# Kernel tuning notes

Measured on AMD Instinct MI355X. Metric: run time of the kernel, lower is better.

Reference implementation:

```python
import jax, jax.numpy as jnp
import numpy as np

E = 200      # embsize
R = 480      # num relations
T = 8        # cur_ts (history length)
N = 40000    # num entities
B = 1024     # batch of triples
NEG_INF = -1.0e9


def _lin(x, W, b):
    # torch nn.Linear convention: y = x @ W.T + b
    return x @ W.T + b


def _gru_cell(x, h, wih, whh, bih, bhh):
    # torch GRUCell: gates packed as [r, z, n]
    gi = x @ wih.T + bih
    gh = h @ whh.T + bhh
    i_r, i_z, i_n = jnp.split(gi, 3, axis=1)
    h_r, h_z, h_n = jnp.split(gh, 3, axis=1)
    r = jax.nn.sigmoid(i_r + h_r)
    z = jax.nn.sigmoid(i_z + h_z)
    n = jnp.tanh(i_n + r * h_n)
    return (1.0 - z) * n + z * h


def setup_inputs() -> dict:
    key = jax.random.key(0)
    ks = jax.random.split(key, 24)
    s = 0.05
    pre_emb = jax.random.normal(ks[0], (N, E), dtype=jnp.float32)
    r_emb = jax.random.normal(ks[1], (R, E), dtype=jnp.float32)
    partial_embeding = jax.random.randint(ks[2], (B, T * R), 0, 2).astype(jnp.float32)
    sub = jax.random.randint(ks[3], (B,), 0, N)
    rel = jax.random.randint(ks[4], (B,), 0, R)
    obj = jax.random.randint(ks[5], (B,), 0, N)
    all_triples = jnp.stack([sub, rel, obj], axis=1).astype(jnp.int64)
    params = {
        'W1': jax.random.normal(ks[6], (2 * E, E)) * s, 'b1': jnp.zeros((2 * E,)),
        'W2': jax.random.normal(ks[7], (E, 2 * E)) * s, 'b2': jnp.zeros((E,)),
        'Wa': jax.random.normal(ks[8], (E, E)) * s, 'ba': jnp.zeros((E,)),
        'Wh1': jax.random.normal(ks[9], (E, E)) * s, 'bh1': jnp.zeros((E,)),
        'Wh2': jax.random.normal(ks[10], (E, E)) * s, 'bh2': jnp.zeros((E,)),
        'Wal': jax.random.normal(ks[11], (E, E)) * s, 'bal': jnp.zeros((E,)),
        'gru_wih': jax.random.normal(ks[12], (3 * E, E)) * s,
        'gru_whh': jax.random.normal(ks[13], (3 * E, E)) * s,
        'gru_bih': jnp.zeros((3 * E,)),
        'gru_bhh': jnp.zeros((3 * E,)),
    }
    params = {k: v.astype(jnp.float32) for k, v in params.items()}
    out = {'pre_emb': pre_emb, 'r_emb': r_emb, 'partial_embeding': partial_embeding,
           'all_triples': all_triples, 'cur_ts': T, 'num_rel': R}
    out.update(params)
    return out


def reference(pre_emb, r_emb, partial_embeding, all_triples, cur_ts, num_rel,
              W1, b1, W2, b2, Wa, ba, Wh1, bh1, Wh2, bh2, Wal, bal,
              gru_wih, gru_whh, gru_bih, gru_bhh):
    mapped_rel = _lin(_lin(r_emb, W1, b1), W2, b2)          # [R, E]
    q_rel = mapped_rel[all_triples[:, 1]]                    # [B, E]
    b = partial_embeding.shape[0]

    # loop-invariant attention base: linear_attn(q_rel) @ mapped_rel^T -> [B, R]
    base = _lin(q_rel, Wa, ba) @ mapped_rel.T

    # [B, cur_ts*R] -> [cur_ts, B, R] for scan over timesteps
    pe = partial_embeding.reshape(b, cur_ts, num_rel).transpose(1, 0, 2)

    def step(h, cur):
        attn = cur * base
        attn = jnp.where(attn == 0, jnp.float32(NEG_INF), attn)
        a = jax.nn.softmax(attn, axis=1)
        x = a @ mapped_rel                                   # [B, E]
        h = _gru_cell(x, h, gru_wih, gru_whh, gru_bih, gru_bhh)
        return h, None

    h0 = jnp.zeros((b, mapped_rel.shape[1]), dtype=pre_emb.dtype)
    gru_hidden, _ = jax.lax.scan(step, h0, pe)

    predicted_hist = 0.1 * _lin(_lin(q_rel, Wh1, bh1), Wh2, bh2) + q_rel
    match_loss = jnp.mean((predicted_hist - gru_hidden) ** 2)

    # forward_forth (distmult scoring)
    gru_hidden2 = _gru_cell(q_rel, predicted_hist, gru_wih, gru_whh, gru_bih, gru_bhh)
    sub_emb = pre_emb[all_triples[:, 0]]
    score_logits = (_lin(sub_emb, Wal, bal) * gru_hidden2) @ _lin(pre_emb, Wal, bal).T  # [B, N]
    score = jax.nn.sigmoid(score_logits)

    labels = jnp.zeros_like(score_logits).at[jnp.arange(b), all_triples[:, 2]].set(1.0)
    # stable BCE(sigmoid(s), y)
    path_loss = -jnp.mean(labels * jax.nn.log_sigmoid(score_logits)
                          + (1.0 - labels) * jax.nn.log_sigmoid(-score_logits))
    return (match_loss, path_loss, score)
```

## Files before the change

kernel.cpp:

```cpp
#include <hip/hip_runtime.h>
#include <hip/hip_bf16.h>
#include <math.h>

#define EE 200
#define RR 480
#define TT 8
#define NN 40000
#define BB 1024
#define KP 224
#define GP 672
#define GPR 704
#define LDS_STRIDE 232
#define SPAN 800

typedef __attribute__((ext_vector_type(8))) short short8v;
typedef __attribute__((ext_vector_type(4))) float f32x4;

__device__ inline unsigned short f2bf(float x) {
    unsigned int u = __float_as_uint(x);
    unsigned int r = ((u >> 16) & 1u) + 0x7fffu;
    return (unsigned short)((u + r) >> 16);
}
__device__ inline float bf2f(unsigned short h) {
    return __uint_as_float(((unsigned int)h) << 16);
}
__device__ inline float sigm(float x) { return 1.0f / (1.0f + __expf(-x)); }
__device__ inline void split_store(unsigned short* hi, unsigned short* lo, size_t i, float v) {
    unsigned short h = f2bf(v);
    hi[i] = h;
    lo[i] = f2bf(v - bf2f(h));
}

struct PrepPtrs {
    unsigned short *W1h, *W1l, *W2h, *W2l, *Wabh, *Wabl, *Wh2h, *Wh2l;
    unsigned short *Walh, *Wall, *WTh, *WTl, *wgh, *wgl, *whg, *whl;
    float *bab, *bihp, *bhhp;
    unsigned short *mapSh, *mapSl, *wgiSh, *wgiSl, *hbufs;
    double* acc;
};

__global__ __launch_bounds__(256) void prep_kernel(
    const float* __restrict__ W1, const float* __restrict__ W2,
    const float* __restrict__ Wa, const float* __restrict__ Wh1,
    const float* __restrict__ Wh2, const float* __restrict__ Wal,
    const float* __restrict__ bal, const float* __restrict__ wih,
    const float* __restrict__ whh, const float* __restrict__ ba,
    const float* __restrict__ bh1, const float* __restrict__ bih,
    const float* __restrict__ bhh, PrepPtrs p)
{
    const int gt = blockIdx.x * 256 + threadIdx.x;
    const int gs = gridDim.x * 256;

    for (int i = gt; i < 448 * 224; i += gs) {
        int r = i / 224, c = i - r * 224;
        split_store(p.W1h, p.W1l, i, (r < 400 && c < 200) ? W1[r * 200 + c] : 0.f);
        float vab = 0.f;
        if (c < 200) {
            if (r < 200) vab = Wa[r * 200 + c];
            else if (r >= 224 && r < 424) vab = Wh1[(r - 224) * 200 + c];
        }
        split_store(p.Wabh, p.Wabl, i, vab);
    }
    for (int i = gt; i < 256 * 416; i += gs) {
        int r = i / 416, c = i - r * 416;
        split_store(p.W2h, p.W2l, i, (r < 200 && c < 400) ? W2[r * 400 + c] : 0.f);
    }
    for (int i = gt; i < 256 * 224; i += gs) {
        int r = i / 224, c = i - r * 224;
        bool in = (r < 200 && c < 200);
        split_store(p.Wh2h, p.Wh2l, i, in ? Wh2[r * 200 + c] : 0.f);
        split_store(p.Walh, p.Wall, i, in ? Wal[r * 200 + c] : 0.f);
        float vt = in ? Wal[c * 200 + r] : ((r == 200 && c < 200) ? bal[c] : 0.f);
        split_store(p.WTh, p.WTl, i, vt);
    }
    for (int i = gt; i < 672 * 224; i += gs) {
        int rr = i / 224, c = i - rr * 224;
        int g = rr / 224, j = rr - g * 224;
        bool in = (j < 200 && c < 200);
        split_store(p.wgh, p.wgl, i, in ? wih[(size_t)(g * 200 + j) * 200 + c] : 0.f);
        split_store(p.whg, p.whl, i, in ? whh[(size_t)(g * 200 + j) * 200 + c] : 0.f);
    }
    for (int i = gt; i < 448; i += gs) {
        float v = 0.f;
        if (i < 200) v = ba[i];
        else if (i >= 224 && i < 424) v = bh1[i - 224];
        p.bab[i] = v;
    }
    for (int i = gt; i < GPR; i += gs) {
        int g = i / 224, j = i - g * 224;
        p.bihp[i] = (g < 3 && j < 200) ? bih[g * 200 + j] : 0.f;
    }
    for (int i = gt; i < GP; i += gs) {
        int g = i / 224, j = i - g * 224;
        p.bhhp[i] = (j < 200) ? bhh[g * 200 + j] : 0.f;
    }
    for (int i = gt; i < 512 * 224; i += gs) { p.mapSh[i] = 0; p.mapSl[i] = 0; }
    for (int i = gt; i < 704 * 480; i += gs) { p.wgiSh[i] = 0; p.wgiSl[i] = 0; }
    for (int i = gt; i < 4 * BB * KP; i += gs) p.hbufs[i] = 0;
    if (gt == 0) { p.acc[0] = 0.0; p.acc[1] = 0.0; }
}

template <int MODE, int OUT, int GATHER, int GATEPAD, int EGATHER>
__global__ __launch_bounds__(256) void mfma_flyA(
    const float* __restrict__ A, int lda, const int* __restrict__ gidx, int gsel,
    const unsigned short* __restrict__ Bhi, const unsigned short* __restrict__ Blo,
    const float* __restrict__ bias,
    float* __restrict__ Cf, unsigned short* __restrict__ Chi, unsigned short* __restrict__ Clo,
    int M, int N, int Ka, int Ks,
    const float* __restrict__ extra, int eld, float alpha, int obf)
{
    const int tid = threadIdx.x;
    const int wave = tid >> 6, lane = tid & 63;
    const int r16 = lane & 15, kq = lane >> 4;
    const int kbase = kq * 8;
    const int bm = blockIdx.y * 64 + wave * 16;
    const int bn = blockIdx.x * 64;

    int arow = bm + r16;
    const bool avalid = arow < M;
    if (GATHER) { if (avalid) arow = gidx[arow * 3 + gsel]; }
    const float* Ap = A + (size_t)arow * lda;

    f32x4 acc[4] = {{0,0,0,0},{0,0,0,0},{0,0,0,0},{0,0,0,0}};
    const int nk = Ks >> 5;

    for (int kk = 0; kk < nk; kk++) {
        const int k0 = kk * 32 + kbase;
        short8v a0, a1;
        #pragma unroll
        for (int e = 0; e < 8; e++) {
            float v = (avalid && (k0 + e) < Ka) ? Ap[k0 + e] : 0.f;
            unsigned short h = f2bf(v);
            a0[e] = (short)h;
            a1[e] = (short)f2bf(v - bf2f(h));
        }
        #pragma unroll
        for (int nf = 0; nf < 4; nf++) {
            const size_t boff = (size_t)(bn + nf * 16 + r16) * Ks + k0;
            short8v b0 = *(const short8v*)(Bhi + boff);
            short8v b1 = *(const short8v*)(Blo + boff);
            acc[nf] = __builtin_amdgcn_mfma_f32_16x16x32_bf16(a0, b1, acc[nf], 0, 0, 0);
            acc[nf] = __builtin_amdgcn_mfma_f32_16x16x32_bf16(a1, b0, acc[nf], 0, 0, 0);
            acc[nf] = __builtin_amdgcn_mfma_f32_16x16x32_bf16(a0, b0, acc[nf], 0, 0, 0);
        }
    }

    #pragma unroll
    for (int r = 0; r < 4; r++) {
        const int orow = bm + kq * 4 + r;
        if (orow >= M) continue;
        #pragma unroll
        for (int nf = 0; nf < 4; nf++) {
            const int col = bn + nf * 16 + r16;
            float v = acc[nf][r];
            if (OUT == 0) {
                if (col < N) {
                    if (bias) v += bias[col];
                    if (MODE == 1) {
                        float ex = EGATHER ? extra[(size_t)gidx[orow * 3 + gsel] * eld + col]
                                           : extra[(size_t)orow * eld + col];
                        v = alpha * v + ex;
                    } else if (MODE == 2) {
                        v = v * extra[(size_t)orow * eld + col];
                    }
                    Cf[(size_t)orow * N + col] = v;
                }
            } else if (OUT == 1) {
                if (col < obf) {
                    float w = 0.f;
                    if (col < N) { w = v; if (bias) w += bias[col]; }
                    Chi[(size_t)orow * obf + col] = f2bf(w);
                }
            } else if (OUT == 2) {
                if (col < N) {
                    int wr = GATEPAD ? (orow / 200) * 224 + orow % 200 : orow;
                    if (bias) v += bias[col];
                    split_store(Chi, Clo, (size_t)wr * obf + col, v);
                }
            } else if (OUT == 3) {
                if (col < N) {
                    if (bias) v += bias[col];
                    Cf[(size_t)orow * N + col] = v;
                    split_store(Chi, Clo, (size_t)orow * obf + col, v);
                }
            }
        }
    }
}

__global__ __launch_bounds__(256) void mfma_linear1_kernel(
    const unsigned short* __restrict__ Ahi,
    const unsigned short* __restrict__ Bhi,
    const float* __restrict__ bias, float* __restrict__ C,
    int M, int N, int Ks)
{
    const int tid  = threadIdx.x;
    const int wave = tid >> 6;
    const int lane = tid & 63;
    const int r16   = lane & 15;
    const int khalf = lane >> 4;
    const int kbase = khalf * 8;
    const int bm = blockIdx.y * 64 + wave * 16;
    const int bn = blockIdx.x * 64;

    const unsigned short* ah = Ahi + (size_t)(bm + r16) * Ks + kbase;
    const unsigned short* bh = Bhi + (size_t)(bn + r16) * Ks + kbase;

    f32x4 acc[4] = {{0,0,0,0},{0,0,0,0},{0,0,0,0},{0,0,0,0}};

    for (int k0 = 0; k0 < Ks; k0 += 32) {
        short8v a0 = *(const short8v*)(ah + k0);
        #pragma unroll
        for (int nf = 0; nf < 4; nf++) {
            short8v b0 = *(const short8v*)(bh + (size_t)nf * 16 * Ks + k0);
            acc[nf] = __builtin_amdgcn_mfma_f32_16x16x32_bf16(a0, b0, acc[nf], 0, 0, 0);
        }
    }
    #pragma unroll
    for (int r = 0; r < 4; r++) {
        const int row = bm + khalf * 4 + r;
        #pragma unroll
        for (int nf = 0; nf < 4; nf++) {
            const int col = bn + nf * 16 + r16;
            if (col < N)
                C[(size_t)row * N + col] = acc[nf][r] + (bias ? bias[col] : 0.0f);
        }
    }
}

template <int FIRST, int LAST>
__global__ __launch_bounds__(256) void gru_step_kernel(
    const unsigned short* __restrict__ Whi, const unsigned short* __restrict__ Wlo,
    const float* __restrict__ bhh_pad,
    const float* __restrict__ gi_t,
    const unsigned short* __restrict__ hin_hi, const unsigned short* __restrict__ hin_lo,
    unsigned short* __restrict__ hout_hi, unsigned short* __restrict__ hout_lo,
    float* __restrict__ h_fin)
{
    const int tid = threadIdx.x;
    const int wave = tid >> 6, lane = tid & 63;
    const int r16 = lane & 15, kq = lane >> 4;
    const int jf = blockIdx.x;
    const int brow = (blockIdx.y * 4 + wave) * 16;
    const int j = jf * 16 + r16;

    f32x4 ar = {0,0,0,0}, az = {0,0,0,0}, an = {0,0,0,0};
    if (!FIRST) {
        short8v ahi[7], alo[7];
        const unsigned short* hh = hin_hi + (size_t)(brow + r16) * KP + kq * 8;
        const unsigned short* hl = hin_lo + (size_t)(brow + r16) * KP + kq * 8;
        #pragma unroll
        for (int kk = 0; kk < 7; kk++) {
            ahi[kk] = *(const short8v*)(hh + kk * 32);
            alo[kk] = *(const short8v*)(hl + kk * 32);
        }
        #pragma unroll
        for (int kk = 0; kk < 7; kk++) {
            const size_t rowr = (size_t)(jf * 16 + r16) * KP + kk * 32 + kq * 8;
            const size_t rowz = rowr + (size_t)224 * KP;
            const size_t rown = rowr + (size_t)448 * KP;
            short8v brh = *(const short8v*)(Whi + rowr);
            short8v brl = *(const short8v*)(Wlo + rowr);
            short8v bzh = *(const short8v*)(Whi + rowz);
            short8v bzl = *(const short8v*)(Wlo + rowz);
            short8v bnh = *(const short8v*)(Whi + rown);
            short8v bnl = *(const short8v*)(Wlo + rown);
            ar = __builtin_amdgcn_mfma_f32_16x16x32_bf16(ahi[kk], brl, ar, 0, 0, 0);
            az = __builtin_amdgcn_mfma_f32_16x16x32_bf16(ahi[kk], bzl, az, 0, 0, 0);
            an = __builtin_amdgcn_mfma_f32_16x16x32_bf16(ahi[kk], bnl, an, 0, 0, 0);
            ar = __builtin_amdgcn_mfma_f32_16x16x32_bf16(alo[kk], brh, ar, 0, 0, 0);
            az = __builtin_amdgcn_mfma_f32_16x16x32_bf16(alo[kk], bzh, az, 0, 0, 0);
            an = __builtin_amdgcn_mfma_f32_16x16x32_bf16(alo[kk], bnh, an, 0, 0, 0);
            ar = __builtin_amdgcn_mfma_f32_16x16x32_bf16(ahi[kk], brh, ar, 0, 0, 0);
            az = __builtin_amdgcn_mfma_f32_16x16x32_bf16(ahi[kk], bzh, az, 0, 0, 0);
            an = __builtin_amdgcn_mfma_f32_16x16x32_bf16(ahi[kk], bnh, an, 0, 0, 0);
        }
    }

    const float br = bhh_pad[j], bz = bhh_pad[224 + j], bn_ = bhh_pad[448 + j];
    #pragma unroll
    for (int q = 0; q < 4; q++) {
        const int row = brow + kq * 4 + q;
        float gir = gi_t[(size_t)row * GP + j];
        float giz = gi_t[(size_t)row * GP + 224 + j];
        float gin = gi_t[(size_t)row * GP + 448 + j];
        float r_ = sigm(gir + ar[q] + br);
        float z_ = sigm(giz + az[q] + bz);
        float n_ = tanhf(gin + r_ * (an[q] + bn_));
        float hold = 0.0f;
        if (!FIRST)
            hold = bf2f(hin_hi[(size_t)row * KP + j]) + bf2f(hin_lo[(size_t)row * KP + j]);
        float hnew = (1.0f - z_) * n_ + z_ * hold;
        if (j < EE) {
            unsigned short nh = f2bf(hnew);
            hout_hi[(size_t)row * KP + j] = nh;
            hout_lo[(size_t)row * KP + j] = f2bf(hnew - bf2f(nh));
            if (LAST) h_fin[(size_t)row * EE + j] = hnew;
        }
    }
}

__global__ __launch_bounds__(256) void gru2_fused_kernel(
    const unsigned short* __restrict__ Wihi, const unsigned short* __restrict__ Wilo,
    const unsigned short* __restrict__ Whhi, const unsigned short* __restrict__ Whlo,
    const float* __restrict__ bih_pad, const float* __restrict__ bhh_pad,
    const int* __restrict__ triples, const float* __restrict__ map,
    const float* __restrict__ hp, const float* __restrict__ hfin,
    float* __restrict__ ghid2, double* __restrict__ accMatch)
{
    __shared__ float red[256];
    const int tid = threadIdx.x;
    const int wave = tid >> 6, lane = tid & 63;
    const int r16 = lane & 15, kq = lane >> 4;
    const int jf = blockIdx.x;
    const int brow = (blockIdx.y * 4 + wave) * 16;
    const int j = jf * 16 + r16;

    f32x4 ir = {0,0,0,0}, iz = {0,0,0,0}, in_ = {0,0,0,0};
    f32x4 hr = {0,0,0,0}, hz = {0,0,0,0}, hn = {0,0,0,0};

    {
        const int xrow = triples[(brow + r16) * 3 + 1];
        const float* xp = map + (size_t)xrow * EE;
        #pragma unroll
        for (int kk = 0; kk < 7; kk++) {
            short8v a0, a1;
            #pragma unroll
            for (int e = 0; e < 8; e++) {
                int k = kk * 32 + kq * 8 + e;
                float v = (k < EE) ? xp[k] : 0.0f;
                unsigned short hhh = f2bf(v);
                a0[e] = (short)hhh;
                a1[e] = (short)f2bf(v - bf2f(hhh));
            }
            const size_t rowr = (size_t)(jf * 16 + r16) * KP + kk * 32 + kq * 8;
            const size_t rowz = rowr + (size_t)224 * KP;
            const size_t rown = rowr + (size_t)448 * KP;
            short8v brh = *(const short8v*)(Wihi + rowr);
            short8v brl = *(const short8v*)(Wilo + rowr);
            short8v bzh = *(const short8v*)(Wihi + rowz);
            short8v bzl = *(const short8v*)(Wilo + rowz);
            short8v bnh = *(const short8v*)(Wihi + rown);
            short8v bnl = *(const short8v*)(Wilo + rown);
            ir = __builtin_amdgcn_mfma_f32_16x16x32_bf16(a0, brl, ir, 0, 0, 0);
            iz = __builtin_amdgcn_mfma_f32_16x16x32_bf16(a0, bzl, iz, 0, 0, 0);
            in_ = __builtin_amdgcn_mfma_f32_16x16x32_bf16(a0, bnl, in_, 0, 0, 0);
            ir = __builtin_amdgcn_mfma_f32_16x16x32_bf16(a1, brh, ir, 0, 0, 0);
            iz = __builtin_amdgcn_mfma_f32_16x16x32_bf16(a1, bzh, iz, 0, 0, 0);
            in_ = __builtin_amdgcn_mfma_f32_16x16x32_bf16(a1, bnh, in_, 0, 0, 0);
            ir = __builtin_amdgcn_mfma_f32_16x16x32_bf16(a0, brh, ir, 0, 0, 0);
            iz = __builtin_amdgcn_mfma_f32_16x16x32_bf16(a0, bzh, iz, 0, 0, 0);
            in_ = __builtin_amdgcn_mfma_f32_16x16x32_bf16(a0, bnh, in_, 0, 0, 0);
        }
    }
    {
        const float* hpp = hp + (size_t)(brow + r16) * EE;
        #pragma unroll
        for (int kk = 0; kk < 7; kk++) {
            short8v a0, a1;
            #pragma unroll
            for (int e = 0; e < 8; e++) {
                int k = kk * 32 + kq * 8 + e;
                float v = (k < EE) ? hpp[k] : 0.0f;
                unsigned short hhh = f2bf(v);
                a0[e] = (short)hhh;
                a1[e] = (short)f2bf(v - bf2f(hhh));
            }
            const size_t rowr = (size_t)(jf * 16 + r16) * KP + kk * 32 + kq * 8;
            const size_t rowz = rowr + (size_t)224 * KP;
            const size_t rown = rowr + (size_t)448 * KP;
            short8v brh = *(const short8v*)(Whhi + rowr);
            short8v brl = *(const short8v*)(Whlo + rowr);
            short8v bzh = *(const short8v*)(Whhi + rowz);
            short8v bzl = *(const short8v*)(Whlo + rowz);
            short8v bnh = *(const short8v*)(Whhi + rown);
            short8v bnl = *(const short8v*)(Whlo + rown);
            hr = __builtin_amdgcn_mfma_f32_16x16x32_bf16(a0, brl, hr, 0, 0, 0);
            hz = __builtin_amdgcn_mfma_f32_16x16x32_bf16(a0, bzl, hz, 0, 0, 0);
            hn = __builtin_amdgcn_mfma_f32_16x16x32_bf16(a0, bnl, hn, 0, 0, 0);
            hr = __builtin_amdgcn_mfma_f32_16x16x32_bf16(a1, brh, hr, 0, 0, 0);
            hz = __builtin_amdgcn_mfma_f32_16x16x32_bf16(a1, bzh, hz, 0, 0, 0);
            hn = __builtin_amdgcn_mfma_f32_16x16x32_bf16(a1, bnh, hn, 0, 0, 0);
            hr = __builtin_amdgcn_mfma_f32_16x16x32_bf16(a0, brh, hr, 0, 0, 0);
            hz = __builtin_amdgcn_mfma_f32_16x16x32_bf16(a0, bzh, hz, 0, 0, 0);
            hn = __builtin_amdgcn_mfma_f32_16x16x32_bf16(a0, bnh, hn, 0, 0, 0);
        }
    }

    float psum = 0.0f;
    if (j < EE) {
        const float bir = bih_pad[j], biz = bih_pad[224 + j], bin = bih_pad[448 + j];
        const float bhr = bhh_pad[j], bhz = bhh_pad[224 + j], bhn = bhh_pad[448 + j];
        #pragma unroll
        for (int q = 0; q < 4; q++) {
            const int row = brow + kq * 4 + q;
            float r_ = sigm(ir[q] + bir + hr[q] + bhr);
            float z_ = sigm(iz[q] + biz + hz[q] + bhz);
            float n_ = tanhf(in_[q] + bin + r_ * (hn[q] + bhn));
            float hold = hp[(size_t)row * EE + j];
            ghid2[(size_t)row * EE + j] = (1.0f - z_) * n_ + z_ * hold;
            float d = hold - hfin[(size_t)row * EE + j];
            psum += d * d;
        }
    }
    red[tid] = psum;
    __syncthreads();
    for (int s = 128; s > 0; s >>= 1) {
        if (tid < s) red[tid] += red[tid + s];
        __syncthreads();
    }
    if (tid == 0) atomicAdd(accMatch, (double)red[0]);
}

__global__ __launch_bounds__(256) void score_mfma3_kernel(
    const unsigned short* __restrict__ Ubf,
    const float* __restrict__ pre_emb,
    const int* __restrict__ triples,
    float* __restrict__ outScore,
    double* __restrict__ accPath)
{
    __shared__ unsigned short Bs[32 * LDS_STRIDE];
    __shared__ int objs[64];
    __shared__ float red[256];

    const int tid = threadIdx.x;
    const int wave = tid >> 6, lane = tid & 63;
    const int r16 = lane & 15, khalf = lane >> 4;
    const int kbase = khalf * 8;
    const int colbase = blockIdx.x * SPAN;
    const int mbase = blockIdx.y * 64;
    const int m0 = mbase + wave * 16;

    if (tid < 64) objs[tid] = triples[(mbase + tid) * 3 + 2];
    for (int idx = tid; idx < 32 * 24; idx += 256) {
        int row = idx / 24;
        int cc = idx - row * 24;
        Bs[row * LDS_STRIDE + 200 + cc] = (cc == 0) ? (unsigned short)0x3F80 : (unsigned short)0;
    }

    short8v a[7];
    {
        const unsigned short* Ap = Ubf + (size_t)(m0 + r16) * KP + kbase;
        #pragma unroll
        for (int kk = 0; kk < 7; kk++) a[kk] = *(const short8v*)(Ap + kk * 32);
    }

    float psum = 0.0f;

    for (int cj = 0; cj < SPAN / 32; cj++) {
        const int bn = colbase + cj * 32;
        __syncthreads();
        for (int idx = tid; idx < 32 * 50; idx += 256) {
            int row = idx / 50;
            int c4 = (idx - row * 50) * 4;
            float4 v = *(const float4*)(pre_emb + (size_t)(bn + row) * EE + c4);
            unsigned short* d = &Bs[row * LDS_STRIDE + c4];
            d[0] = f2bf(v.x); d[1] = f2bf(v.y); d[2] = f2bf(v.z); d[3] = f2bf(v.w);
        }
        __syncthreads();

        f32x4 acc0 = {0,0,0,0}, acc1 = {0,0,0,0};
        #pragma unroll
        for (int kk = 0; kk < 7; kk++) {
            short8v b0 = *(const short8v*)&Bs[( 0 + r16) * LDS_STRIDE + kk * 32 + kbase];
            short8v b1 = *(const short8v*)&Bs[(16 + r16) * LDS_STRIDE + kk * 32 + kbase];
            acc0 = __builtin_amdgcn_mfma_f32_16x16x32_bf16(a[kk], b0, acc0, 0, 0, 0);
            acc1 = __builtin_amdgcn_mfma_f32_16x16x32_bf16(a[kk], b1, acc1, 0, 0, 0);
        }
        #pragma unroll
        for (int r = 0; r < 4; r++) {
            const int grow = m0 + khalf * 4 + r;
            const int objc = objs[grow - mbase];
            float xv[2] = { acc0[r], acc1[r] };
            #pragma unroll
            for (int nf = 0; nf < 2; nf++) {
                const int col = bn + nf * 16 + r16;
                float x  = xv[nf];
                float e  = __expf(-fabsf(x));
                float t1 = 1.0f + e;
                float rc = __builtin_amdgcn_rcpf(t1);
                float sig = (x >= 0.0f) ? rc : e * rc;
                float sp = __logf(t1);
                float s  = (col == objc) ? x : -x;
                psum += fminf(s, 0.0f) - sp;
                outScore[(size_t)grow * NN + col] = sig;
            }
        }
    }
    red[tid] = psum;
    __syncthreads();
    for (int s = 128; s > 0; s >>= 1) {
        if (tid < s) red[tid] += red[tid + s];
        __syncthreads();
    }
    if (tid == 0) atomicAdd(accPath, (double)red[0]);
}

__global__ __launch_bounds__(256) void masked_softmax_all_kernel(
    const float* __restrict__ base, const float* __restrict__ part,
    unsigned short* __restrict__ aout_hi)
{
    __shared__ float sv[RR];
    __shared__ float red[256];
    const int blk = blockIdx.x;
    const int b = blk & (BB - 1);
    const int t = blk >> 10;
    const int tid = threadIdx.x;
    const float* brow = base + (size_t)b * RR;
    const float* prow = part + (size_t)b * (TT * RR) + t * RR;

    float lmax = -3.0e38f;
    for (int r = tid; r < RR; r += 256) {
        float v = prow[r] * brow[r];
        if (v == 0.0f) v = -1000000000.0f;
        sv[r] = v;
        lmax = fmaxf(lmax, v);
    }
    red[tid] = lmax;
    __syncthreads();
    for (int s = 128; s > 0; s >>= 1) {
        if (tid < s) red[tid] = fmaxf(red[tid], red[tid + s]);
        __syncthreads();
    }
    float gmax = red[0];
    __syncthreads();

    float lsum = 0.0f;
    for (int r = tid; r < RR; r += 256) {
        float e = __expf(sv[r] - gmax);
        sv[r] = e;
        lsum += e;
    }
    red[tid] = lsum;
    __syncthreads();
    for (int s = 128; s > 0; s >>= 1) {
        if (tid < s) red[tid] += red[tid + s];
        __syncthreads();
    }
    float inv = 1.0f / red[0];
    for (int r = tid; r < RR; r += 256)
        aout_hi[(size_t)blk * RR + r] = f2bf(sv[r] * inv);
}

__global__ void final_kernel(const double* __restrict__ acc, float* __restrict__ out)
{
    if (threadIdx.x == 0) {
        out[0] = (float)(acc[0] / ((double)BB * EE));
        out[1] = (float)(-acc[1] / ((double)BB * NN));
    }
}

extern "C" void kernel_launch(void* const* d_in, const int* in_sizes, int n_in,
                              void* d_out, int out_size, void* d_ws, size_t ws_size,
                              hipStream_t stream) {
    const float* pre_emb = (const float*)d_in[0];
    const float* r_emb   = (const float*)d_in[1];
    const float* part    = (const float*)d_in[2];
    const int*   triples = (const int*)d_in[3];
    const float* W1  = (const float*)d_in[6];
    const float* b1  = (const float*)d_in[7];
    const float* W2  = (const float*)d_in[8];
    const float* b2  = (const float*)d_in[9];
    const float* Wa  = (const float*)d_in[10];
    const float* ba  = (const float*)d_in[11];
    const float* Wh1 = (const float*)d_in[12];
    const float* bh1 = (const float*)d_in[13];
    const float* Wh2 = (const float*)d_in[14];
    const float* bh2 = (const float*)d_in[15];
    const float* Wal = (const float*)d_in[16];
    const float* bal = (const float*)d_in[17];
    const float* wih = (const float*)d_in[18];
    const float* whh = (const float*)d_in[19];
    const float* bih = (const float*)d_in[20];
    const float* bhh = (const float*)d_in[21];

    float* out = (float*)d_out;
    double* acc = (double*)d_ws;
    float* wsf = (float*)d_ws;
    size_t off = 4;
    auto alloc = [&](size_t n) { float* p = wsf + off; off += (n + 3) & ~(size_t)3; return p; };
    auto allocS = [&](size_t n) { return (unsigned short*)alloc((n + 1) / 2); };

    PrepPtrs p;
    p.W1h  = allocS((size_t)448 * 224);
    p.W1l  = allocS((size_t)448 * 224);
    p.W2h  = allocS((size_t)256 * 416);
    p.W2l  = allocS((size_t)256 * 416);
    p.Wabh = allocS((size_t)448 * 224);
    p.Wabl = allocS((size_t)448 * 224);
    p.Wh2h = allocS((size_t)256 * 224);
    p.Wh2l = allocS((size_t)256 * 224);
    p.Walh = allocS((size_t)256 * 224);
    p.Wall = allocS((size_t)256 * 224);
    p.WTh  = allocS((size_t)256 * 224);
    p.WTl  = allocS((size_t)256 * 224);
    p.wgh  = allocS((size_t)GP * KP);
    p.wgl  = allocS((size_t)GP * KP);
    p.whg  = allocS((size_t)GP * KP);
    p.whl  = allocS((size_t)GP * KP);
    p.bab  = alloc(448);
    p.bihp = alloc(GPR);
    p.bhhp = alloc(GP);
    p.mapSh = allocS((size_t)512 * 224);
    p.mapSl = allocS((size_t)512 * 224);
    p.wgiSh = allocS((size_t)GPR * RR);
    p.wgiSl = allocS((size_t)GPR * RR);
    p.hbufs = allocS((size_t)4 * BB * KP);
    p.acc = acc;

    unsigned short* ha_hi = p.hbufs;
    unsigned short* ha_lo = p.hbufs + (size_t)BB * KP;
    unsigned short* hb_hi = p.hbufs + (size_t)2 * BB * KP;
    unsigned short* hb_lo = p.hbufs + (size_t)3 * BB * KP;

    float* h1     = alloc((size_t)RR * 400);
    float* map    = alloc((size_t)RR * EE);
    float* qa_ph1 = alloc((size_t)BB * 448);
    float* basep  = alloc((size_t)BB * RR);
    unsigned short* aw_hi = allocS((size_t)TT * BB * RR);
    float* gi_all = alloc((size_t)TT * BB * GP);
    float* hfin   = alloc((size_t)BB * EE);
    float* pred   = alloc((size_t)BB * EE);
    float* ghid2  = alloc((size_t)BB * EE);
    float* s1h    = alloc((size_t)BB * EE);
    unsigned short* u_bf = allocS((size_t)BB * KP);

    dim3 blk(256);

    prep_kernel<<<1024, blk, 0, stream>>>(
        W1, W2, Wa, Wh1, Wh2, Wal, bal, wih, whh, ba, bh1, bih, bhh, p);

    mfma_flyA<0,0,0,0,0><<<dim3(7, 8), blk, 0, stream>>>(
        r_emb, 200, nullptr, 0, p.W1h, p.W1l, b1, h1, nullptr, nullptr,
        RR, 400, 200, 224, nullptr, 0, 0.f, 0);
    mfma_flyA<0,3,0,0,0><<<dim3(4, 8), blk, 0, stream>>>(
        h1, 400, nullptr, 0, p.W2h, p.W2l, b2, map, p.mapSh, p.mapSl,
        RR, EE, 400, 416, nullptr, 0, 0.f, 224);
    mfma_flyA<0,0,1,0,0><<<dim3(7, 16), blk, 0, stream>>>(
        map, 200, triples, 1, p.Wabh, p.Wabl, p.bab, qa_ph1, nullptr, nullptr,
        BB, 448, 200, 224, nullptr, 0, 0.f, 0);
    mfma_flyA<0,0,0,0,0><<<dim3(8, 16), blk, 0, stream>>>(
        qa_ph1, 448, nullptr, 0, p.mapSh, p.mapSl, nullptr, basep, nullptr, nullptr,
        BB, RR, 200, 224, nullptr, 0, 0.f, 0);
    masked_softmax_all_kernel<<<TT * BB, blk, 0, stream>>>(basep, part, aw_hi);
    mfma_flyA<0,2,0,1,0><<<dim3(8, 10), blk, 0, stream>>>(
        wih, 200, nullptr, 0, p.mapSh, p.mapSl, nullptr, nullptr, p.wgiSh, p.wgiSl,
        600, RR, 200, 224, nullptr, 0, 0.f, RR);
    mfma_linear1_kernel<<<dim3(11, TT * BB / 64), blk, 0, stream>>>(
        aw_hi, p.wgiSh, p.bihp, gi_all, TT * BB, GP, RR);

    for (int t = 0; t < TT; t++) {
        const float* gi_t = gi_all + (size_t)t * BB * GP;
        const unsigned short* ih = (t & 1) ? hb_hi : ha_hi;
        const unsigned short* il = (t & 1) ? hb_lo : ha_lo;
        unsigned short* oh = (t & 1) ? ha_hi : hb_hi;
        unsigned short* ol = (t & 1) ? ha_lo : hb_lo;
        if (t == 0)
            gru_step_kernel<1,0><<<dim3(13, BB / 64), blk, 0, stream>>>(
                p.whg, p.whl, p.bhhp, gi_t, ih, il, oh, ol, nullptr);
        else if (t == TT - 1)
            gru_step_kernel<0,1><<<dim3(13, BB / 64), blk, 0, stream>>>(
                p.whg, p.whl, p.bhhp, gi_t, ih, il, oh, ol, hfin);
        else
            gru_step_kernel<0,0><<<dim3(13, BB / 64), blk, 0, stream>>>(
                p.whg, p.whl, p.bhhp, gi_t, ih, il, oh, ol, nullptr);
    }

    mfma_flyA<1,0,0,0,1><<<dim3(4, 16), blk, 0, stream>>>(
        qa_ph1 + 224, 448, triples, 1, p.Wh2h, p.Wh2l, bh2, pred, nullptr, nullptr,
        BB, EE, 200, 224, map, 200, 0.1f, 0);
    gru2_fused_kernel<<<dim3(13, BB / 64), blk, 0, stream>>>(
        p.wgh, p.wgl, p.whg, p.whl, p.bihp, p.bhhp,
        triples, map, pred, hfin, ghid2, acc + 0);
    mfma_flyA<2,0,1,0,0><<<dim3(4, 16), blk, 0, stream>>>(
        pre_emb, 200, triples, 0, p.Walh, p.Wall, bal, s1h, nullptr, nullptr,
        BB, EE, 200, 224, ghid2, 200, 0.f, 0);
    mfma_flyA<0,1,0,0,0><<<dim3(4, 16), blk, 0, stream>>>(
        s1h, 200, nullptr, 0, p.WTh, p.WTl, nullptr, nullptr, u_bf, nullptr,
        BB, KP, 200, 224, nullptr, 0, 0.f, KP);
    score_mfma3_kernel<<<dim3(50, 16), blk, 0, stream>>>(u_bf, pre_emb, triples, out + 2, acc + 1);
    final_kernel<<<1, 64, 0, stream>>>(acc, out);
}
```

Baseline: 457.2 us.

## Swap MFMA operand roles in score kernel to write rows with float4 stores

The score GEMM kernel is restructured so pre_emb rows become the A operand, loaded straight from global memory and converted to bf16 in registers instead of being staged through LDS. U becomes the B operand, held in registers. The transposed output layout lets each lane store four consecutive columns of its own row as one float4, which is meant to improve write coalescing on the large 1024x40000 score output. LDS staging and the per-tile barriers are removed and the grid doubles. The trade-off is that pre_emb is now read redundantly by every wave with no LDS sharing, and each block covers a shorter column span.

After: 581.4 us. 1.27x slower.

```diff
diff --git a/kernel.cpp b/kernel.cpp
--- a/kernel.cpp
+++ b/kernel.cpp
@@ -10,8 +10,6 @@
 #define KP 224
 #define GP 672
 #define GPR 704
-#define LDS_STRIDE 232
-#define SPAN 800
 
 typedef __attribute__((ext_vector_type(8))) short short8v;
 typedef __attribute__((ext_vector_type(4))) float f32x4;
@@ -412,81 +410,77 @@
     if (tid == 0) atomicAdd(accMatch, (double)red[0]);
 }
 
-__global__ __launch_bounds__(256) void score_mfma3_kernel(
+__global__ __launch_bounds__(256) void score_mfma4_kernel(
     const unsigned short* __restrict__ Ubf,
     const float* __restrict__ pre_emb,
     const int* __restrict__ triples,
     float* __restrict__ outScore,
     double* __restrict__ accPath)
 {
-    __shared__ unsigned short Bs[32 * LDS_STRIDE];
-    __shared__ int objs[64];
     __shared__ float red[256];
-
     const int tid = threadIdx.x;
     const int wave = tid >> 6, lane = tid & 63;
-    const int r16 = lane & 15, khalf = lane >> 4;
-    const int kbase = khalf * 8;
-    const int colbase = blockIdx.x * SPAN;
-    const int mbase = blockIdx.y * 64;
-    const int m0 = mbase + wave * 16;
-
-    if (tid < 64) objs[tid] = triples[(mbase + tid) * 3 + 2];
-    for (int idx = tid; idx < 32 * 24; idx += 256) {
-        int row = idx / 24;
-        int cc = idx - row * 24;
-        Bs[row * LDS_STRIDE + 200 + cc] = (cc == 0) ? (unsigned short)0x3F80 : (unsigned short)0;
-    }
-
-    short8v a[7];
+    const int r16 = lane & 15, kq = lane >> 4;
+    const int kbase = kq * 8;
+    const int pc = blockIdx.x * 400;
+    const int u0 = blockIdx.y * 64 + wave * 16;
+
+    short8v bU[7];
     {
-        const unsigned short* Ap = Ubf + (size_t)(m0 + r16) * KP + kbase;
-        #pragma unroll
-        for (int kk = 0; kk < 7; kk++) a[kk] = *(const short8v*)(Ap + kk * 32);
-    }
+        const unsigned short* Up = Ubf + (size_t)(u0 + r16) * KP + kbase;
+        #pragma unroll
+        for (int kk = 0; kk < 7; kk++) bU[kk] = *(const short8v*)(Up + kk * 32);
+    }
+    const int myUrow = u0 + r16;
+    const int objc = triples[myUrow * 3 + 2];
 
     float psum = 0.0f;
 
-    for (int cj = 0; cj < SPAN / 32; cj++) {
-        const int bn = colbase + cj * 32;
-        __syncthreads();
-        for (int idx = tid; idx < 32 * 50; idx += 256) {
-            int row = idx / 50;
-            int c4 = (idx - row * 50) * 4;
-            float4 v = *(const float4*)(pre_emb + (size_t)(bn + row) * EE + c4);
-            unsigned short* d = &Bs[row * LDS_STRIDE + c4];
-            d[0] = f2bf(v.x); d[1] = f2bf(v.y); d[2] = f2bf(v.z); d[3] = f2bf(v.w);
-        }
-        __syncthreads();
-
-        f32x4 acc0 = {0,0,0,0}, acc1 = {0,0,0,0};
+    #pragma unroll
+    for (int m = 0; m < 25; m++) {
+        const int prow = pc + m * 16 + r16;
+        const float* Pp = pre_emb + (size_t)prow * EE;
+        f32x4 acc = {0, 0, 0, 0};
         #pragma unroll
         for (int kk = 0; kk < 7; kk++) {
-            short8v b0 = *(const short8v*)&Bs[( 0 + r16) * LDS_STRIDE + kk * 32 + kbase];
-            short8v b1 = *(const short8v*)&Bs[(16 + r16) * LDS_STRIDE + kk * 32 + kbase];
-            acc0 = __builtin_amdgcn_mfma_f32_16x16x32_bf16(a[kk], b0, acc0, 0, 0, 0);
-            acc1 = __builtin_amdgcn_mfma_f32_16x16x32_bf16(a[kk], b1, acc1, 0, 0, 0);
-        }
+            short8v a;
+            if (kk < 6) {
+                const float* src = Pp + kk * 32 + kbase;
+                float4 v0 = *(const float4*)(src);
+                float4 v1 = *(const float4*)(src + 4);
+                a[0] = (short)f2bf(v0.x); a[1] = (short)f2bf(v0.y);
+                a[2] = (short)f2bf(v0.z); a[3] = (short)f2bf(v0.w);
+                a[4] = (short)f2bf(v1.x); a[5] = (short)f2bf(v1.y);
+                a[6] = (short)f2bf(v1.z); a[7] = (short)f2bf(v1.w);
+            } else {
+                #pragma unroll
+                for (int e = 0; e < 8; e++) {
+                    int k = 192 + kq * 8 + e;
+                    float v = (k < EE) ? Pp[k] : ((k == EE) ? 1.0f : 0.0f);
+                    a[e] = (short)f2bf(v);
+                }
+            }
+            acc = __builtin_amdgcn_mfma_f32_16x16x32_bf16(a, bU[kk], acc, 0, 0, 0);
+        }
+        const int cbase = pc + m * 16 + kq * 4;
+        float4 ov;
+        float* op = (float*)&ov;
         #pragma unroll
         for (int r = 0; r < 4; r++) {
-            const int grow = m0 + khalf * 4 + r;
-            const int objc = objs[grow - mbase];
-            float xv[2] = { acc0[r], acc1[r] };
-            #pragma unroll
-            for (int nf = 0; nf < 2; nf++) {
-                const int col = bn + nf * 16 + r16;
-                float x  = xv[nf];
-                float e  = __expf(-fabsf(x));
-                float t1 = 1.0f + e;
-                float rc = __builtin_amdgcn_rcpf(t1);
-                float sig = (x >= 0.0f) ? rc : e * rc;
-                float sp = __logf(t1);
-                float s  = (col == objc) ? x : -x;
-                psum += fminf(s, 0.0f) - sp;
-                outScore[(size_t)grow * NN + col] = sig;
-            }
-        }
-    }
+            const int col = cbase + r;
+            float x  = acc[r];
+            float e  = __expf(-fabsf(x));
+            float t1 = 1.0f + e;
+            float rc = __builtin_amdgcn_rcpf(t1);
+            float sig = (x >= 0.0f) ? rc : e * rc;
+            float sp = __logf(t1);
+            float s  = (col == objc) ? x : -x;
+            psum += fminf(s, 0.0f) - sp;
+            op[r] = sig;
+        }
+        *(float4*)&outScore[(size_t)myUrow * NN + cbase] = ov;
+    }
+
     red[tid] = psum;
     __syncthreads();
     for (int s = 128; s > 0; s >>= 1) {
@@ -678,6 +672,6 @@
     mfma_flyA<0,1,0,0,0><<<dim3(4, 16), blk, 0, stream>>>(
         s1h, 200, nullptr, 0, p.WTh, p.WTl, nullptr, nullptr, u_bf, nullptr,
         BB, KP, 200, 224, nullptr, 0, 0.f, KP);
-    score_mfma3_kernel<<<dim3(50, 16), blk, 0, stream>>>(u_bf, pre_emb, triples, out + 2, acc + 1);
+    score_mfma4_kernel<<<dim3(100, 16), blk, 0, stream>>>(u_bf, pre_emb, triples, out + 2, acc + 1);
     final_kernel<<<1, 64, 0, stream>>>(acc, out);
 }
```
